# Optimization experiments

Measured on AMD Instinct MI355X. Metric: run time of the kernel, lower is better.

Reference implementation:

```python
import jax, jax.numpy as jnp
import numpy as np

K = 2  # kernel_size implied by the output view (s3-1, s4-1, s5-1) with padding=0, stride=1


def setup_inputs() -> dict:
    key = jax.random.key(0)
    kx, kw = jax.random.split(key)
    B, C, D, H, W = 8, 16, 64, 64, 64
    O = 32
    x = jax.random.normal(kx, (B, C, D, H, W), dtype=jnp.float32)
    w = jax.random.normal(kw, (O, C * K * K * K), dtype=jnp.float32) * 0.05
    return {"x": x, "w": w}


def reference(x, w):
    # unfoldNd (im2col, C-major then kd,kh,kw) followed by einsum('ij,kjm->kim', w, y)
    # is exactly a VALID 3D convolution with kernel w.reshape(O, C, K, K, K).
    B, C, D, H, W = x.shape
    O = w.shape[0]
    kernel = w.reshape(O, C, K, K, K)
    y = jax.lax.conv_general_dilated(
        x, kernel,
        window_strides=(1, 1, 1),
        padding='VALID',
        dimension_numbers=('NCDHW', 'OIDHW', 'NCDHW'),
    )  # (B, O, D-1, H-1, W-1)
    return (y + 1.0) ** 2
```

## Files before the change

### kernel.cpp

```cpp
#include <hip/hip_runtime.h>
#include <hip/hip_bf16.h>


typedef __attribute__((ext_vector_type(8)))  short short8;
typedef __attribute__((ext_vector_type(4)))  float f32x4;
typedef __attribute__((ext_vector_type(16))) float f32x16;
typedef __attribute__((ext_vector_type(4)))  unsigned short u16x4;

#define XCS 262144
#define OS  250047
#define SLAB_E 9216
#define KH8_E  4608
#define IMG_DW 536

__device__ __forceinline__ unsigned short f2bf(float f) {
    unsigned int u = __builtin_bit_cast(unsigned int, f);
    return (unsigned short)((u + 0x7fffu + ((u >> 16) & 1u)) >> 16);
}

__global__ __launch_bounds__(256, 4) void conv3d_k2_line(
    const float* __restrict__ x,
    const float* __restrict__ wgt,
    float* __restrict__ out)
{
    __shared__ __align__(16) unsigned char lds_raw[40960];
    unsigned short* tile  = (unsigned short*)lds_raw;
    unsigned short* strip = (unsigned short*)(lds_raw + 36864);
    float* img = (float*)lds_raw;

    const int t   = threadIdx.x;
    const int l   = t & 63;
    const int wv  = t >> 6;
    const int col = l & 31;
    const int kh8 = l >> 5;

    const int h0 = blockIdx.x * 8;
    const int d  = blockIdx.y;
    const int b  = blockIdx.z;

    short8 aF[8];
    {
        f32x4 wreg[16];
        const float* wp = wgt + col * 128 + kh8 * 64;
#pragma unroll
        for (int q = 0; q < 16; ++q) wreg[q] = *(const f32x4*)(wp + q * 4);
#pragma unroll
        for (int tap = 0; tap < 8; ++tap) {
            short8 a;
#pragma unroll
            for (int j = 0; j < 8; ++j) {
                const int k = j * 8 + tap;
                a[j] = (short)f2bf(wreg[k >> 2][k & 3]);
            }
            aF[tap] = a;
        }
    }

    const int cA   = t >> 4;
    const int wq   = t & 15;
    const int wB   = l;
    const int kh8s = wv >> 1;
    const int half = wv & 1;

    f32x4 v[2][9];
#pragma unroll
    for (int p = 0; p < 2; ++p) {
        const float* xs = x + (size_t)b * 16 * XCS + (size_t)(d + p) * 4096
                            + (size_t)cA * XCS + wq * 4;
#pragma unroll
        for (int h = 0; h < 9; ++h) {
            int hp = h0 + h; if (hp > 63) hp = 63;
            v[p][h] = *(const f32x4*)(xs + hp * 64);
        }
    }

#pragma unroll
    for (int p = 0; p < 2; ++p) {
#pragma unroll
        for (int h = 0; h < 9; ++h) {
            unsigned short* sb = strip + (h & 1) * 1024;
            u16x4 pk;
#pragma unroll
            for (int i = 0; i < 4; ++i) pk[i] = f2bf(v[p][h][i]);
            *(u16x4*)&sb[cA * 64 + wq * 4] = pk;
            u16x4 q;
#pragma unroll
            for (int i = 0; i < 4; ++i)
                q[i] = sb[(wv * 4 + i) * 64 + wB];
            *(u16x4*)&tile[p * SLAB_E + kh8s * KH8_E + h * 512 + wB * 8 + half * 4] = q;
        }
    }
    __syncthreads();

    f32x16 acc[2][2];
#pragma unroll
    for (int th = 0; th < 2; ++th) {
        const int hl = wv * 2 + th;
#pragma unroll
        for (int wh = 0; wh < 2; ++wh) {
            const int wb = wh * 32;
            f32x16 a = {};
#pragma unroll
            for (int kd = 0; kd < 2; ++kd)
#pragma unroll
            for (int kh = 0; kh < 2; ++kh)
#pragma unroll
            for (int kw = 0; kw < 2; ++kw) {
                const int tap = kd * 4 + kh * 2 + kw;
                short8 bfrag = *(const short8*)&tile[kd * SLAB_E + kh8 * KH8_E
                    + (hl + kh) * 512 + (wb + col + kw) * 8];
                a = __builtin_amdgcn_mfma_f32_32x32x16_bf16(aF[tap], bfrag, a, 0, 0, 0);
            }
            acc[th][wh] = a;
        }
    }
    __syncthreads();

    const int hvalid = (h0 == 56) ? 7 : 8;
    const int runlen = hvalid * 63;
#pragma unroll
    for (int p = 0; p < 2; ++p) {
#pragma unroll
        for (int th = 0; th < 2; ++th) {
            const int hl = wv * 2 + th;
            if (hl < hvalid) {
#pragma unroll
                for (int wh = 0; wh < 2; ++wh) {
                    const int wc = wh * 32 + col;
                    if (wc < 63) {
#pragma unroll
                        for (int r = 0; r < 8; ++r) {
                            const int rr = p * 8 + r;
                            const int og = (rr & 3) + 8 * (rr >> 2) + 4 * kh8;
                            const int ol = og - p * 16;
                            const int sh = (int)(((unsigned)(d - og - h0 + 1024)) & 31u);
                            float y = acc[th][wh][rr] + 1.0f;
                            img[ol * IMG_DW + sh + hl * 63 + wc] = y * y;
                        }
                    }
                }
            }
        }
        __syncthreads();
#pragma unroll
        for (int orun = 0; orun < 4; ++orun) {
            const int ol = wv * 4 + orun;
            const int og = p * 16 + ol;
            const size_t base_dw = ((size_t)b * 32 + og) * (size_t)OS
                                 + (size_t)d * 3969 + (size_t)h0 * 63;
            float* gp = out + base_dw;
            const int sh = (int)(base_dw & 31);
            const float* ip = img + ol * IMG_DW + sh;
            int hc = (32 - sh) & 31;
            if (hc > runlen) hc = runlen;
            if (l < hc) gp[l] = ip[l];
            const int ni = ((runlen - hc) >> 5) << 5;
            const int nv = ni >> 2;
#pragma unroll
            for (int rnd = 0; rnd < 2; ++rnd) {
                const int k = rnd * 64 + l;
                if (k < nv) {
                    f32x4 qv = *(const f32x4*)(ip + hc + 4 * k);
                    __builtin_nontemporal_store(qv, (f32x4*)(gp + hc + 4 * k));
                }
            }
            const int ts = hc + ni;
            if (ts + l < runlen) gp[ts + l] = ip[ts + l];
        }
        if (p == 0) __syncthreads();
    }
}

extern "C" void kernel_launch(void* const* d_in, const int* in_sizes, int n_in,
                              void* d_out, int out_size, void* d_ws, size_t ws_size,
                              hipStream_t stream) {
    const float* x   = (const float*)d_in[0];
    const float* wgt = (const float*)d_in[1];
    float* out = (float*)d_out;

    dim3 grid(8, 63, 8);
    dim3 block(256);
    conv3d_k2_line<<<grid, block, 0, stream>>>(x, wgt, out);
}
```

Baseline: 76.79 us.

## Transpose input tile in registers instead of via LDS strip buffer

The input staging is reworked so each thread loads four channels for one (h,w) quad and transposes channel-to-inner order in registers. The result is written straight into a padded tile layout (channel-innermost with row stride 1040) instead of bouncing through an LDS strip. This removes the extra LDS round trip and its serialization. It also splits the loads so that the halo row is fetched while the first rows are being converted. The cost is more live registers and a different LDS bank pattern for the MFMA B-fragment reads.

```diff
diff --git a/kernel.cpp b/kernel.cpp
--- a/kernel.cpp
+++ b/kernel.cpp
@@ -9,8 +9,8 @@
 
 #define XCS 262144
 #define OS  250047
-#define SLAB_E 9216
-#define KH8_E  4608
+#define HST 1040
+#define PST 9360
 #define IMG_DW 536
 
 __device__ __forceinline__ unsigned short f2bf(float f) {
@@ -18,14 +18,13 @@
     return (unsigned short)((u + 0x7fffu + ((u >> 16) & 1u)) >> 16);
 }
 
-__global__ __launch_bounds__(256, 4) void conv3d_k2_line(
+__global__ __launch_bounds__(256, 4) void conv3d_k2_regT(
     const float* __restrict__ x,
     const float* __restrict__ wgt,
     float* __restrict__ out)
 {
-    __shared__ __align__(16) unsigned char lds_raw[40960];
-    unsigned short* tile  = (unsigned short*)lds_raw;
-    unsigned short* strip = (unsigned short*)(lds_raw + 36864);
+    __shared__ __align__(16) unsigned char lds_raw[37440];
+    unsigned short* tile = (unsigned short*)lds_raw;
     float* img = (float*)lds_raw;
 
     const int t   = threadIdx.x;
@@ -56,39 +55,69 @@
         }
     }
 
-    const int cA   = t >> 4;
-    const int wq   = t & 15;
-    const int wB   = l;
-    const int kh8s = wv >> 1;
-    const int half = wv & 1;
-
-    f32x4 v[2][9];
-#pragma unroll
-    for (int p = 0; p < 2; ++p) {
-        const float* xs = x + (size_t)b * 16 * XCS + (size_t)(d + p) * 4096
-                            + (size_t)cA * XCS + wq * 4;
-#pragma unroll
-        for (int h = 0; h < 9; ++h) {
-            int hp = h0 + h; if (hp > 63) hp = 63;
-            v[p][h] = *(const f32x4*)(xs + hp * 64);
-        }
-    }
-
-#pragma unroll
-    for (int p = 0; p < 2; ++p) {
-#pragma unroll
-        for (int h = 0; h < 9; ++h) {
-            unsigned short* sb = strip + (h & 1) * 1024;
+    const int hsub = l >> 4;
+    const int scq  = (l >> 2) & 3;
+    const int wq   = wv * 4 + (l & 3);
+    const float* xb = x + (size_t)b * 16 * XCS;
+
+    f32x4 v[4][4];
+#pragma unroll
+    for (int rd = 0; rd < 4; ++rd) {
+        const int p  = rd >> 1;
+        const int hq = rd & 1;
+        const float* xs = xb + (size_t)(d + p) * 4096
+                             + (h0 + hq * 4 + hsub) * 64 + wq * 4;
+#pragma unroll
+        for (int i = 0; i < 4; ++i)
+            v[rd][i] = *(const f32x4*)(xs + (size_t)(scq * 4 + i) * XCS);
+    }
+
+#pragma unroll
+    for (int rd = 0; rd < 2; ++rd) {
+        const int p = rd >> 1, hq = rd & 1, h = hq * 4 + hsub;
+#pragma unroll
+        for (int i = 0; i < 4; ++i) {
             u16x4 pk;
 #pragma unroll
-            for (int i = 0; i < 4; ++i) pk[i] = f2bf(v[p][h][i]);
-            *(u16x4*)&sb[cA * 64 + wq * 4] = pk;
-            u16x4 q;
+            for (int j = 0; j < 4; ++j) pk[j] = f2bf(v[rd][j][i]);
+            *(u16x4*)&tile[p * PST + h * HST + (wq * 4 + i) * 16 + scq * 4] = pk;
+        }
+    }
+
+    f32x4 vt[2][4];
+    int hp8 = h0 + 8; if (hp8 > 63) hp8 = 63;
+    if (hsub == 0) {
+#pragma unroll
+        for (int p = 0; p < 2; ++p) {
+            const float* xs = xb + (size_t)(d + p) * 4096 + hp8 * 64 + wq * 4;
 #pragma unroll
             for (int i = 0; i < 4; ++i)
-                q[i] = sb[(wv * 4 + i) * 64 + wB];
-            *(u16x4*)&tile[p * SLAB_E + kh8s * KH8_E + h * 512 + wB * 8 + half * 4] = q;
-        }
+                vt[p][i] = *(const f32x4*)(xs + (size_t)(scq * 4 + i) * XCS);
+        }
+    }
+
+#pragma unroll
+    for (int rd = 2; rd < 4; ++rd) {
+        const int p = rd >> 1, hq = rd & 1, h = hq * 4 + hsub;
+#pragma unroll
+        for (int i = 0; i < 4; ++i) {
+            u16x4 pk;
+#pragma unroll
+            for (int j = 0; j < 4; ++j) pk[j] = f2bf(v[rd][j][i]);
+            *(u16x4*)&tile[p * PST + h * HST + (wq * 4 + i) * 16 + scq * 4] = pk;
+        }
+    }
+
+    if (hsub == 0) {
+#pragma unroll
+        for (int p = 0; p < 2; ++p)
+#pragma unroll
+            for (int i = 0; i < 4; ++i) {
+                u16x4 pk;
+#pragma unroll
+                for (int j = 0; j < 4; ++j) pk[j] = f2bf(vt[p][j][i]);
+                *(u16x4*)&tile[p * PST + 8 * HST + (wq * 4 + i) * 16 + scq * 4] = pk;
+            }
     }
     __syncthreads();
 
@@ -107,8 +136,8 @@
 #pragma unroll
             for (int kw = 0; kw < 2; ++kw) {
                 const int tap = kd * 4 + kh * 2 + kw;
-                short8 bfrag = *(const short8*)&tile[kd * SLAB_E + kh8 * KH8_E
-                    + (hl + kh) * 512 + (wb + col + kw) * 8];
+                short8 bfrag = *(const short8*)&tile[kd * PST
+                    + (hl + kh) * HST + (wb + col + kw) * 16 + kh8 * 8];
                 a = __builtin_amdgcn_mfma_f32_32x32x16_bf16(aF[tap], bfrag, a, 0, 0, 0);
             }
             acc[th][wh] = a;
@@ -180,5 +209,5 @@
 
     dim3 grid(8, 63, 8);
     dim3 block(256);
-    conv3d_k2_line<<<grid, block, 0, stream>>>(x, wgt, out);
+    conv3d_k2_regT<<<grid, block, 0, stream>>>(x, wgt, out);
 }
```

Result: slower. 92.63 us (+20.6%).

## Roll each block over four depth slices, reusing bf16 slabs and prefetching

Applied to the files above, without the earlier changes.

Each block now handles up to four consecutive output depth slices instead of one. It keeps two bf16-transposed input slabs in LDS as a rolling buffer, so each input plane is loaded and converted once per block instead of twice, and the next plane is prefetched into registers while MFMA and stores run. The weight-fragment setup is amortised over more work. The epilogue image buffer gets its own LDS region, which nearly doubles LDS per block and lowers the launch-bounds occupancy hint from 4 to 2. The grid shrinks by about four times, which may reduce parallelism and latency hiding.

```diff
diff --git a/kernel.cpp b/kernel.cpp
--- a/kernel.cpp
+++ b/kernel.cpp
@@ -18,15 +18,15 @@
     return (unsigned short)((u + 0x7fffu + ((u >> 16) & 1u)) >> 16);
 }
 
-__global__ __launch_bounds__(256, 4) void conv3d_k2_line(
+__global__ __launch_bounds__(256, 2) void conv3d_k2_rollvec(
     const float* __restrict__ x,
     const float* __restrict__ wgt,
     float* __restrict__ out)
 {
-    __shared__ __align__(16) unsigned char lds_raw[40960];
+    __shared__ __align__(16) unsigned char lds_raw[75264];
     unsigned short* tile  = (unsigned short*)lds_raw;
     unsigned short* strip = (unsigned short*)(lds_raw + 36864);
-    float* img = (float*)lds_raw;
+    float* img = (float*)(lds_raw + 40960);
 
     const int t   = threadIdx.x;
     const int l   = t & 63;
@@ -35,8 +35,9 @@
     const int kh8 = l >> 5;
 
     const int h0 = blockIdx.x * 8;
-    const int d  = blockIdx.y;
+    const int d0 = blockIdx.y * 4;
     const int b  = blockIdx.z;
+    const int nd = (d0 == 60) ? 3 : 4;
 
     short8 aF[8];
     {
@@ -61,113 +62,137 @@
     const int wB   = l;
     const int kh8s = wv >> 1;
     const int half = wv & 1;
-
-    f32x4 v[2][9];
-#pragma unroll
-    for (int p = 0; p < 2; ++p) {
-        const float* xs = x + (size_t)b * 16 * XCS + (size_t)(d + p) * 4096
-                            + (size_t)cA * XCS + wq * 4;
-#pragma unroll
-        for (int h = 0; h < 9; ++h) {
-            int hp = h0 + h; if (hp > 63) hp = 63;
-            v[p][h] = *(const f32x4*)(xs + hp * 64);
-        }
-    }
-
-#pragma unroll
-    for (int p = 0; p < 2; ++p) {
+    const float* xb = x + (size_t)b * 16 * XCS + (size_t)cA * XCS + wq * 4;
+
+    auto xpose = [&](const f32x4* vv, int bufSel) {
 #pragma unroll
         for (int h = 0; h < 9; ++h) {
             unsigned short* sb = strip + (h & 1) * 1024;
             u16x4 pk;
 #pragma unroll
-            for (int i = 0; i < 4; ++i) pk[i] = f2bf(v[p][h][i]);
+            for (int i = 0; i < 4; ++i) pk[i] = f2bf(vv[h][i]);
             *(u16x4*)&sb[cA * 64 + wq * 4] = pk;
             u16x4 q;
 #pragma unroll
             for (int i = 0; i < 4; ++i)
                 q[i] = sb[(wv * 4 + i) * 64 + wB];
-            *(u16x4*)&tile[p * SLAB_E + kh8s * KH8_E + h * 512 + wB * 8 + half * 4] = q;
-        }
+            *(u16x4*)&tile[bufSel * SLAB_E + kh8s * KH8_E + h * 512 + wB * 8 + half * 4] = q;
+        }
+    };
+
+    {
+        f32x4 v0[9], v1[9];
+#pragma unroll
+        for (int h = 0; h < 9; ++h) {
+            int hp = h0 + h; if (hp > 63) hp = 63;
+            v0[h] = *(const f32x4*)(xb + (size_t)d0 * 4096 + hp * 64);
+        }
+#pragma unroll
+        for (int h = 0; h < 9; ++h) {
+            int hp = h0 + h; if (hp > 63) hp = 63;
+            v1[h] = *(const f32x4*)(xb + (size_t)(d0 + 1) * 4096 + hp * 64);
+        }
+        xpose(v0, 0);
+        xpose(v1, 1);
     }
     __syncthreads();
 
-    f32x16 acc[2][2];
-#pragma unroll
-    for (int th = 0; th < 2; ++th) {
-        const int hl = wv * 2 + th;
-#pragma unroll
-        for (int wh = 0; wh < 2; ++wh) {
-            const int wb = wh * 32;
-            f32x16 a = {};
-#pragma unroll
-            for (int kd = 0; kd < 2; ++kd)
-#pragma unroll
-            for (int kh = 0; kh < 2; ++kh)
-#pragma unroll
-            for (int kw = 0; kw < 2; ++kw) {
-                const int tap = kd * 4 + kh * 2 + kw;
-                short8 bfrag = *(const short8*)&tile[kd * SLAB_E + kh8 * KH8_E
-                    + (hl + kh) * 512 + (wb + col + kw) * 8];
-                a = __builtin_amdgcn_mfma_f32_32x32x16_bf16(aF[tap], bfrag, a, 0, 0, 0);
-            }
-            acc[th][wh] = a;
-        }
-    }
-    __syncthreads();
-
     const int hvalid = (h0 == 56) ? 7 : 8;
     const int runlen = hvalid * 63;
-#pragma unroll
-    for (int p = 0; p < 2; ++p) {
+
+    for (int dd = 0; dd < nd; ++dd) {
+        const bool doPre = (dd + 1) < nd;
+
+        f32x4 pre[9];
+        if (doPre) {
+#pragma unroll
+            for (int h = 0; h < 9; ++h) {
+                int hp = h0 + h; if (hp > 63) hp = 63;
+                pre[h] = *(const f32x4*)(xb + (size_t)(d0 + dd + 2) * 4096 + hp * 64);
+            }
+        }
+
+        const int pA = (dd & 1) * SLAB_E;
+        const int pB = ((dd + 1) & 1) * SLAB_E;
+
+        f32x16 acc[2][2];
 #pragma unroll
         for (int th = 0; th < 2; ++th) {
             const int hl = wv * 2 + th;
-            if (hl < hvalid) {
-#pragma unroll
-                for (int wh = 0; wh < 2; ++wh) {
-                    const int wc = wh * 32 + col;
-                    if (wc < 63) {
-#pragma unroll
-                        for (int r = 0; r < 8; ++r) {
-                            const int rr = p * 8 + r;
-                            const int og = (rr & 3) + 8 * (rr >> 2) + 4 * kh8;
-                            const int ol = og - p * 16;
-                            const int sh = (int)(((unsigned)(d - og - h0 + 1024)) & 31u);
-                            float y = acc[th][wh][rr] + 1.0f;
-                            img[ol * IMG_DW + sh + hl * 63 + wc] = y * y;
+#pragma unroll
+            for (int wh = 0; wh < 2; ++wh) {
+                const int wb = wh * 32;
+                f32x16 a = {};
+#pragma unroll
+                for (int kd = 0; kd < 2; ++kd)
+#pragma unroll
+                for (int kh = 0; kh < 2; ++kh)
+#pragma unroll
+                for (int kw = 0; kw < 2; ++kw) {
+                    const int tap = kd * 4 + kh * 2 + kw;
+                    short8 bfrag = *(const short8*)&tile[(kd ? pB : pA)
+                        + kh8 * KH8_E + (hl + kh) * 512 + (wb + col + kw) * 8];
+                    a = __builtin_amdgcn_mfma_f32_32x32x16_bf16(aF[tap], bfrag, a, 0, 0, 0);
+                }
+                acc[th][wh] = a;
+            }
+        }
+
+        const int dcur = d0 + dd;
+#pragma unroll
+        for (int p = 0; p < 2; ++p) {
+#pragma unroll
+            for (int th = 0; th < 2; ++th) {
+                const int hl = wv * 2 + th;
+                if (hl < hvalid) {
+#pragma unroll
+                    for (int wh = 0; wh < 2; ++wh) {
+                        const int wc = wh * 32 + col;
+                        if (wc < 63) {
+#pragma unroll
+                            for (int r = 0; r < 8; ++r) {
+                                const int rr = p * 8 + r;
+                                const int og = (rr & 3) + 8 * (rr >> 2) + 4 * kh8;
+                                const int ol = og - p * 16;
+                                const int sh = (int)(((unsigned)(dcur - og - h0 + 1024)) & 31u);
+                                float y = acc[th][wh][rr] + 1.0f;
+                                img[ol * IMG_DW + sh + hl * 63 + wc] = y * y;
+                            }
                         }
                     }
                 }
             }
-        }
+            __syncthreads();
+#pragma unroll
+            for (int orun = 0; orun < 4; ++orun) {
+                const int ol = wv * 4 + orun;
+                const int og = p * 16 + ol;
+                const size_t base_dw = ((size_t)b * 32 + og) * (size_t)OS
+                                     + (size_t)dcur * 3969 + (size_t)h0 * 63;
+                float* gp = out + base_dw;
+                const int sh = (int)(base_dw & 31);
+                const float* ip = img + ol * IMG_DW + sh;
+                int hc = (32 - sh) & 31;
+                if (hc > runlen) hc = runlen;
+                if (l < hc) gp[l] = ip[l];
+                const int ni = ((runlen - hc) >> 5) << 5;
+                const int nv = ni >> 2;
+#pragma unroll
+                for (int rnd = 0; rnd < 2; ++rnd) {
+                    const int k = rnd * 64 + l;
+                    if (k < nv) {
+                        f32x4 qv = *(const f32x4*)(ip + hc + 4 * k);
+                        __builtin_nontemporal_store(qv, (f32x4*)(gp + hc + 4 * k));
+                    }
+                }
+                const int ts = hc + ni;
+                if (ts + l < runlen) gp[ts + l] = ip[ts + l];
+            }
+            if (p == 0) __syncthreads();
+        }
+
+        if (doPre) xpose(pre, dd & 1);
         __syncthreads();
-#pragma unroll
-        for (int orun = 0; orun < 4; ++orun) {
-            const int ol = wv * 4 + orun;
-            const int og = p * 16 + ol;
-            const size_t base_dw = ((size_t)b * 32 + og) * (size_t)OS
-                                 + (size_t)d * 3969 + (size_t)h0 * 63;
-            float* gp = out + base_dw;
-            const int sh = (int)(base_dw & 31);
-            const float* ip = img + ol * IMG_DW + sh;
-            int hc = (32 - sh) & 31;
-            if (hc > runlen) hc = runlen;
-            if (l < hc) gp[l] = ip[l];
-            const int ni = ((runlen - hc) >> 5) << 5;
-            const int nv = ni >> 2;
-#pragma unroll
-            for (int rnd = 0; rnd < 2; ++rnd) {
-                const int k = rnd * 64 + l;
-                if (k < nv) {
-                    f32x4 qv = *(const f32x4*)(ip + hc + 4 * k);
-                    __builtin_nontemporal_store(qv, (f32x4*)(gp + hc + 4 * k));
-                }
-            }
-            const int ts = hc + ni;
-            if (ts + l < runlen) gp[ts + l] = ip[ts + l];
-        }
-        if (p == 0) __syncthreads();
     }
 }
 
@@ -178,7 +203,7 @@
     const float* wgt = (const float*)d_in[1];
     float* out = (float*)d_out;
 
-    dim3 grid(8, 63, 8);
+    dim3 grid(8, 16, 8);
     dim3 block(256);
-    conv3d_k2_line<<<grid, block, 0, stream>>>(x, wgt, out);
+    conv3d_k2_rollvec<<<grid, block, 0, stream>>>(x, wgt, out);
 }
```

Result: no change. 77.28 us (+0.6%).
